# Kernel optimization log

Hardware: AMD Instinct MI355X
Metric: run time of the kernel (lower is better)

## Reference

```python
import jax, jax.numpy as jnp
import numpy as np

B, S, D = 4, 2048, 4096
E, R, OUT = 4, 64, 4096
NUM_MOD, NUM_REG, HID = 4, 3, 128
ALPHA = 128.0
SCALING = ALPHA / R  # alpha / rank = 2.0
BALANCE_COEFF = 0.01


def setup_inputs() -> dict:
    key = jax.random.key(0)
    ks = jax.random.split(key, 8)
    return {
        "x": jax.random.normal(ks[0], (B, S, D), jnp.float32),
        "reliability_vec": jax.random.uniform(ks[1], (B, NUM_MOD), jnp.float32),
        "regime_vec": jax.random.uniform(ks[2], (B, NUM_REG), jnp.float32),
        # LoRA experts stacked: A ~ N(0, 1/rank), B random (torch inits B=0; randomized here for a non-trivial baseline)
        "lora_A": jax.random.normal(ks[3], (E, R, D), jnp.float32) / np.sqrt(R).astype(np.float32),
        "lora_B": jax.random.normal(ks[4], (E, OUT, R), jnp.float32) * 0.02,
        # router: Linear(4103->128) -> GELU -> Linear(128->4)
        "w1": jax.random.normal(ks[5], (D + NUM_MOD + NUM_REG, HID), jnp.float32) * 0.02,
        "b1": jnp.zeros((HID,), jnp.float32),
        "w2": jax.random.normal(ks[6], (HID, E), jnp.float32) * 0.02,
        "b2": jnp.zeros((E,), jnp.float32),
    }


def reference(x, reliability_vec, regime_vec, lora_A, lora_B, w1, b1, w2, b2):
    # Router on pooled features + degradation context
    x_pooled = x.mean(axis=1)                                   # [B, D]
    router_in = jnp.concatenate([x_pooled, reliability_vec, regime_vec], axis=-1)
    h = jax.nn.gelu(router_in @ w1 + b1)                        # [B, HID]
    gate_logits = h @ w2 + b2                                   # [B, E]
    gate_probs = jax.nn.softmax(gate_logits, axis=-1)
    top_expert = jnp.argmax(gate_probs, axis=-1)                # [B] int

    # Sparse top-1 dispatch (eval path): gather each sample's expert weights
    A_sel = lora_A[top_expert]                                  # [B, R, D]
    B_sel = lora_B[top_expert]                                  # [B, OUT, R]
    xr = jnp.einsum('bsd,brd->bsr', x, A_sel)                   # [B, S, R]
    out = jnp.einsum('bsr,bor->bso', xr, B_sel) * SCALING       # [B, S, OUT]

    avg_gate = gate_probs.mean(axis=0)
    balance_loss = BALANCE_COEFF * (E * jnp.sum(avg_gate ** 2))
    return out, balance_loss
```

## Files before the change

### kernel.cpp

```cpp
#include <hip/hip_runtime.h>

constexpr int B_ = 4, S_ = 2048, D_ = 4096, E_ = 4, R_ = 64, OUT_ = 4096;
constexpr int NMOD = 4, NREG = 3, HID_ = 128;
constexpr int RIN_ = D_ + NMOD + NREG;
constexpr float SCALING_ = 2.0f;
constexpr int P_   = 128;
constexpr int KC_  = 33;

constexpr size_t WS_PP    = 0;
constexpr size_t WS_HACC2 = WS_PP + (size_t)P_ * B_ * D_;
constexpr size_t WS_TOP   = WS_HACC2 + B_ * KC_ * HID_;
constexpr size_t WS_APK   = WS_TOP + 16;
constexpr size_t WS_BPK   = WS_APK + (size_t)E_ * R_ * D_ / 2;

using short8 = __attribute__((ext_vector_type(8))) short;
using f32x4  = __attribute__((ext_vector_type(4))) float;
union frag_u { int4 i4; short8 s8; };

__device__ inline unsigned short f2bf(float f) {
    unsigned u = __float_as_uint(f);
    unsigned r = u + 0x7FFFu + ((u >> 16) & 1u);
    return (unsigned short)(r >> 16);
}

__global__ __launch_bounds__(256) void prep_kernel(const float* __restrict__ x,
                                                   const float* __restrict__ A,
                                                   const float* __restrict__ Bw,
                                                   float* __restrict__ pp,
                                                   ushort* __restrict__ Apk,
                                                   ushort* __restrict__ Bpk) {
    int bx = blockIdx.x, t = threadIdx.x;
    if (bx < 512) {
        int strip = bx >> 2, b = bx & 3;
        const float4* xp = (const float4*)(x + ((size_t)b * S_ + strip * 16) * D_);
        float4 a0 = {0,0,0,0}, a1 = {0,0,0,0}, a2 = {0,0,0,0}, a3 = {0,0,0,0};
#pragma unroll 4
        for (int r = 0; r < 16; ++r) {
            float4 v0 = xp[(size_t)r * 1024 + t];
            float4 v1 = xp[(size_t)r * 1024 + 256 + t];
            float4 v2 = xp[(size_t)r * 1024 + 512 + t];
            float4 v3 = xp[(size_t)r * 1024 + 768 + t];
            a0.x += v0.x; a0.y += v0.y; a0.z += v0.z; a0.w += v0.w;
            a1.x += v1.x; a1.y += v1.y; a1.z += v1.z; a1.w += v1.w;
            a2.x += v2.x; a2.y += v2.y; a2.z += v2.z; a2.w += v2.w;
            a3.x += v3.x; a3.y += v3.y; a3.z += v3.z; a3.w += v3.w;
        }
        float* ppb = pp + ((size_t)strip * B_ + b) * D_;
        *(float4*)&ppb[(t)       * 4] = a0;
        *(float4*)&ppb[(256 + t) * 4] = a1;
        *(float4*)&ppb[(512 + t) * 4] = a2;
        *(float4*)&ppb[(768 + t) * 4] = a3;
    } else if (bx < 1024) {
        int idx = (bx - 512) * 256 + t;
        int l = idx & 63, n = (idx >> 6) & 3, ks = (idx >> 8) & 127, e = idx >> 15;
        const float* src = A + ((size_t)e * R_ + n * 16 + (l & 15)) * D_
                             + ks * 32 + (l >> 4) * 8;
        float4 v0 = *(const float4*)(src);
        float4 v1 = *(const float4*)(src + 4);
        ushort* dst = Apk + (size_t)idx * 8;
        *(ushort4*)(dst)     = make_ushort4(f2bf(v0.x), f2bf(v0.y), f2bf(v0.z), f2bf(v0.w));
        *(ushort4*)(dst + 4) = make_ushort4(f2bf(v1.x), f2bf(v1.y), f2bf(v1.z), f2bf(v1.w));
    } else {
        int idx = (bx - 1024) * 256 + t;
        int l = idx & 63, kk = (idx >> 6) & 1, nt = (idx >> 7) & 255, e = idx >> 15;
        const float* src = Bw + ((size_t)e * OUT_ + nt * 16 + (l & 15)) * R_
                              + kk * 32 + (l >> 4) * 8;
        float4 v0 = *(const float4*)(src);
        float4 v1 = *(const float4*)(src + 4);
        ushort* dst = Bpk + (size_t)idx * 8;
        *(ushort4*)(dst)     = make_ushort4(f2bf(v0.x), f2bf(v0.y), f2bf(v0.z), f2bf(v0.w));
        *(ushort4*)(dst + 4) = make_ushort4(f2bf(v1.x), f2bf(v1.y), f2bf(v1.z), f2bf(v1.w));
    }
}

__global__ __launch_bounds__(256) void router_h_kernel(const float* __restrict__ pp,
                                                       const float* __restrict__ rel,
                                                       const float* __restrict__ reg,
                                                       const float* __restrict__ w1,
                                                       float* __restrict__ hacc2) {
    __shared__ float rin[128];
    __shared__ float red[256];
    int b = blockIdx.x, kc = blockIdx.y;
    int t = threadIdx.x;
    int k0 = kc * 128;
    {
        int k = k0 + (t & 127), half = t >> 7;
        float s = 0.f;
        if (k < D_) {
            for (int pi = half * 64; pi < half * 64 + 64; ++pi)
                s += pp[((size_t)pi * B_ + b) * D_ + k];
        }
        red[t] = s;
    }
    __syncthreads();
    if (t < 128) {
        int k = k0 + t;
        float v = 0.f;
        if (k < D_)               v = (red[t] + red[t + 128]) * (1.0f / S_);
        else if (k < D_ + NMOD)   v = rel[b * NMOD + (k - D_)];
        else if (k < RIN_)        v = reg[b * NREG + (k - D_ - NMOD)];
        rin[t] = v;
    }
    __syncthreads();
    int h = t & 127, half = t >> 7;
    float acc = 0.f;
#pragma unroll 8
    for (int i = 0; i < 64; ++i) {
        int kk = 2 * i + half;
        int k = k0 + kk;
        if (k < RIN_) acc += rin[kk] * w1[(size_t)k * HID_ + h];
    }
    red[t] = acc;
    __syncthreads();
    if (t < 128)
        hacc2[((size_t)b * KC_ + kc) * HID_ + t] = red[t] + red[t + 128];
}

__global__ void router_finish_kernel(const float* __restrict__ hacc2, const float* __restrict__ b1,
                                     const float* __restrict__ w2, const float* __restrict__ b2,
                                     int* __restrict__ top, float* __restrict__ bal_out) {
    __shared__ float h_lds[B_][HID_];
    __shared__ float logit[B_][E_];
    __shared__ float probs[B_][E_];
    int t = threadIdx.x;
    for (int b = 0; b < B_; ++b) {
        float v = b1[t];
        for (int j = 0; j < KC_; ++j) v += hacc2[((size_t)b * KC_ + j) * HID_ + t];
        float u = 0.7978845608028654f * (v + 0.044715f * v * v * v);
        h_lds[b][t] = 0.5f * v * (1.0f + tanhf(u));
    }
    __syncthreads();
    if (t < B_ * E_) {
        int b = t >> 2, e = t & 3;
        float acc = b2[e];
        for (int j = 0; j < HID_; ++j) acc += h_lds[b][j] * w2[j * E_ + e];
        logit[b][e] = acc;
    }
    __syncthreads();
    if (t < B_) {
        int b = t;
        float mx = logit[b][0]; int arg = 0;
        for (int e = 1; e < E_; ++e) if (logit[b][e] > mx) { mx = logit[b][e]; arg = e; }
        float s = 0.f, pv[E_];
        for (int e = 0; e < E_; ++e) { pv[e] = expf(logit[b][e] - mx); s += pv[e]; }
        for (int e = 0; e < E_; ++e) probs[b][e] = pv[e] / s;
        top[b] = arg;
    }
    __syncthreads();
    if (t == 0) {
        float bal = 0.f;
        for (int e = 0; e < E_; ++e) {
            float avg = 0.25f * (probs[0][e] + probs[1][e] + probs[2][e] + probs[3][e]);
            bal += avg * avg;
        }
        *bal_out = 0.01f * E_ * bal;
    }
}

__global__ __launch_bounds__(512) void xrout_kernel(const float* __restrict__ x,
                                                    const ushort* __restrict__ Apk,
                                                    const ushort* __restrict__ Bpk,
                                                    const int* __restrict__ top,
                                                    float* __restrict__ out) {
    __shared__ ushort xsw[8][16][70];
    __shared__ float  red[4][2][16][68];
    __shared__ ushort xs2[32][70];
    int sb = blockIdx.x, b = blockIdx.y;
    int e  = top[b];
    int s0 = sb * 32;
    int t = threadIdx.x, l = t & 63, w = t >> 6;
    int h = w & 1, ksl = w >> 1;
    int kb = ksl * 1024;

    const float* xb = x + ((size_t)b * S_ + s0 + h * 16) * D_;
    const int4*  ap = (const int4*)Apk + (size_t)e * 128 * 4 * 64 + l;
    f32x4 acc[4] = {};
    int lr = l >> 4, lc = l & 15;
    for (int i = 0; i < 16; ++i) {
        int k0 = kb + i * 64;
        float4 xv[4];
#pragma unroll
        for (int j = 0; j < 4; ++j)
            xv[j] = *(const float4*)(xb + (size_t)(lr + 4 * j) * D_ + k0 + lc * 4);
#pragma unroll
        for (int j = 0; j < 4; ++j)
            *(ushort4*)&xsw[w][lr + 4 * j][lc * 4] =
                make_ushort4(f2bf(xv[j].x), f2bf(xv[j].y), f2bf(xv[j].z), f2bf(xv[j].w));
#pragma unroll
        for (int kk = 0; kk < 2; ++kk) {
            short8 xf = *(const short8*)&xsw[w][l & 15][kk * 32 + (l >> 4) * 8];
            int ksg = ksl * 32 + i * 2 + kk;
#pragma unroll
            for (int n = 0; n < 4; ++n) {
                frag_u af; af.i4 = ap[((size_t)ksg * 4 + n) * 64];
                acc[n] = __builtin_amdgcn_mfma_f32_16x16x32_bf16(xf, af.s8, acc[n], 0, 0, 0);
            }
        }
    }
#pragma unroll
    for (int n = 0; n < 4; ++n)
#pragma unroll
        for (int i = 0; i < 4; ++i)
            red[ksl][h][(l >> 4) * 4 + i][n * 16 + (l & 15)] = acc[n][i];
    __syncthreads();
    {
        int row = t >> 4, c4 = (t & 15) * 4;
        int hh = row >> 4, r16 = row & 15;
        float4 s = *(const float4*)&red[0][hh][r16][c4];
#pragma unroll
        for (int ks = 1; ks < 4; ++ks) {
            float4 r = *(const float4*)&red[ks][hh][r16][c4];
            s.x += r.x; s.y += r.y; s.z += r.z; s.w += r.w;
        }
        *(ushort4*)&xs2[row][c4] = make_ushort4(f2bf(s.x), f2bf(s.y), f2bf(s.z), f2bf(s.w));
    }
    __syncthreads();

    short8 xf2[2][2];
#pragma unroll
    for (int m = 0; m < 2; ++m)
#pragma unroll
        for (int kk = 0; kk < 2; ++kk)
            xf2[m][kk] = *(const short8*)&xs2[m * 16 + (l & 15)][kk * 32 + (l >> 4) * 8];
    const int4* bp = (const int4*)Bpk + (size_t)e * 256 * 2 * 64 + l;
    float* ob = out + ((size_t)b * S_ + s0) * OUT_ + w * 512;
    int ro = (l >> 4) * 4, co = l & 15;
#pragma unroll 4
    for (int ntl = 0; ntl < 32; ++ntl) {
        int nt = w * 32 + ntl;
        frag_u bf0, bf1;
        bf0.i4 = bp[((size_t)nt * 2 + 0) * 64];
        bf1.i4 = bp[((size_t)nt * 2 + 1) * 64];
        f32x4 a2[2] = {};
#pragma unroll
        for (int m = 0; m < 2; ++m) {
            a2[m] = __builtin_amdgcn_mfma_f32_16x16x32_bf16(xf2[m][0], bf0.s8, a2[m], 0, 0, 0);
            a2[m] = __builtin_amdgcn_mfma_f32_16x16x32_bf16(xf2[m][1], bf1.s8, a2[m], 0, 0, 0);
        }
#pragma unroll
        for (int m = 0; m < 2; ++m)
#pragma unroll
            for (int i = 0; i < 4; ++i)
                ob[(size_t)(m * 16 + ro + i) * OUT_ + ntl * 16 + co] = a2[m][i] * SCALING_;
    }
}

extern "C" void kernel_launch(void* const* d_in, const int* in_sizes, int n_in,
                              void* d_out, int out_size, void* d_ws, size_t ws_size,
                              hipStream_t stream) {
    const float* x   = (const float*)d_in[0];
    const float* rel = (const float*)d_in[1];
    const float* reg = (const float*)d_in[2];
    const float* lA  = (const float*)d_in[3];
    const float* lB  = (const float*)d_in[4];
    const float* w1  = (const float*)d_in[5];
    const float* b1  = (const float*)d_in[6];
    const float* w2  = (const float*)d_in[7];
    const float* b2  = (const float*)d_in[8];
    float* out = (float*)d_out;
    float* ws  = (float*)d_ws;

    float*  pp    = ws + WS_PP;
    float*  hacc2 = ws + WS_HACC2;
    int*    top   = (int*)(ws + WS_TOP);
    ushort* Apk   = (ushort*)(ws + WS_APK);
    ushort* Bpk   = (ushort*)(ws + WS_BPK);

    prep_kernel<<<1536, 256, 0, stream>>>(x, lA, lB, pp, Apk, Bpk);
    router_h_kernel<<<dim3(B_, KC_), 256, 0, stream>>>(pp, rel, reg, w1, hacc2);
    router_finish_kernel<<<1, 128, 0, stream>>>(hacc2, b1, w2, b2, top,
                                                out + (size_t)out_size - 1);
    xrout_kernel<<<dim3(S_ / 32, B_), 512, 0, stream>>>(x, Apk, Bpk, top, out);
}
```

Before: 113.3 us.

## Shrink xrout row tile to 16 and split K across all eight waves

```diff
diff --git a/kernel.cpp b/kernel.cpp
--- a/kernel.cpp
+++ b/kernel.cpp
@@ -163,20 +163,19 @@
                                                     const int* __restrict__ top,
                                                     float* __restrict__ out) {
     __shared__ ushort xsw[8][16][70];
-    __shared__ float  red[4][2][16][68];
-    __shared__ ushort xs2[32][70];
+    __shared__ float  red[8][16][68];
+    __shared__ ushort xs2[16][70];
     int sb = blockIdx.x, b = blockIdx.y;
     int e  = top[b];
-    int s0 = sb * 32;
+    int s0 = sb * 16;
     int t = threadIdx.x, l = t & 63, w = t >> 6;
-    int h = w & 1, ksl = w >> 1;
-    int kb = ksl * 1024;
-
-    const float* xb = x + ((size_t)b * S_ + s0 + h * 16) * D_;
+    int kb = w * 512;
+
+    const float* xb = x + ((size_t)b * S_ + s0) * D_;
     const int4*  ap = (const int4*)Apk + (size_t)e * 128 * 4 * 64 + l;
     f32x4 acc[4] = {};
     int lr = l >> 4, lc = l & 15;
-    for (int i = 0; i < 16; ++i) {
+    for (int i = 0; i < 8; ++i) {
         int k0 = kb + i * 64;
         float4 xv[4];
 #pragma unroll
@@ -189,7 +188,7 @@
 #pragma unroll
         for (int kk = 0; kk < 2; ++kk) {
             short8 xf = *(const short8*)&xsw[w][l & 15][kk * 32 + (l >> 4) * 8];
-            int ksg = ksl * 32 + i * 2 + kk;
+            int ksg = w * 16 + i * 2 + kk;
 #pragma unroll
             for (int n = 0; n < 4; ++n) {
                 frag_u af; af.i4 = ap[((size_t)ksg * 4 + n) * 64];
@@ -201,27 +200,25 @@
     for (int n = 0; n < 4; ++n)
 #pragma unroll
         for (int i = 0; i < 4; ++i)
-            red[ksl][h][(l >> 4) * 4 + i][n * 16 + (l & 15)] = acc[n][i];
+            red[w][(l >> 4) * 4 + i][n * 16 + (l & 15)] = acc[n][i];
     __syncthreads();
     {
-        int row = t >> 4, c4 = (t & 15) * 4;
-        int hh = row >> 4, r16 = row & 15;
-        float4 s = *(const float4*)&red[0][hh][r16][c4];
-#pragma unroll
-        for (int ks = 1; ks < 4; ++ks) {
-            float4 r = *(const float4*)&red[ks][hh][r16][c4];
-            s.x += r.x; s.y += r.y; s.z += r.z; s.w += r.w;
-        }
-        *(ushort4*)&xs2[row][c4] = make_ushort4(f2bf(s.x), f2bf(s.y), f2bf(s.z), f2bf(s.w));
-    }
-    __syncthreads();
-
-    short8 xf2[2][2];
-#pragma unroll
-    for (int m = 0; m < 2; ++m)
-#pragma unroll
-        for (int kk = 0; kk < 2; ++kk)
-            xf2[m][kk] = *(const short8*)&xs2[m * 16 + (l & 15)][kk * 32 + (l >> 4) * 8];
+        int row = t >> 5, c2 = (t & 31) * 2;
+        float s0f = red[0][row][c2], s1f = red[0][row][c2 + 1];
+#pragma unroll
+        for (int ks = 1; ks < 8; ++ks) {
+            s0f += red[ks][row][c2];
+            s1f += red[ks][row][c2 + 1];
+        }
+        xs2[row][c2]     = f2bf(s0f);
+        xs2[row][c2 + 1] = f2bf(s1f);
+    }
+    __syncthreads();
+
+    short8 xf2[2];
+#pragma unroll
+    for (int kk = 0; kk < 2; ++kk)
+        xf2[kk] = *(const short8*)&xs2[l & 15][kk * 32 + (l >> 4) * 8];
     const int4* bp = (const int4*)Bpk + (size_t)e * 256 * 2 * 64 + l;
     float* ob = out + ((size_t)b * S_ + s0) * OUT_ + w * 512;
     int ro = (l >> 4) * 4, co = l & 15;
@@ -231,17 +228,12 @@
         frag_u bf0, bf1;
         bf0.i4 = bp[((size_t)nt * 2 + 0) * 64];
         bf1.i4 = bp[((size_t)nt * 2 + 1) * 64];
-        f32x4 a2[2] = {};
-#pragma unroll
-        for (int m = 0; m < 2; ++m) {
-            a2[m] = __builtin_amdgcn_mfma_f32_16x16x32_bf16(xf2[m][0], bf0.s8, a2[m], 0, 0, 0);
-            a2[m] = __builtin_amdgcn_mfma_f32_16x16x32_bf16(xf2[m][1], bf1.s8, a2[m], 0, 0, 0);
-        }
-#pragma unroll
-        for (int m = 0; m < 2; ++m)
-#pragma unroll
-            for (int i = 0; i < 4; ++i)
-                ob[(size_t)(m * 16 + ro + i) * OUT_ + ntl * 16 + co] = a2[m][i] * SCALING_;
+        f32x4 a2 = {};
+        a2 = __builtin_amdgcn_mfma_f32_16x16x32_bf16(xf2[0], bf0.s8, a2, 0, 0, 0);
+        a2 = __builtin_amdgcn_mfma_f32_16x16x32_bf16(xf2[1], bf1.s8, a2, 0, 0, 0);
+#pragma unroll
+        for (int i = 0; i < 4; ++i)
+            ob[(size_t)(ro + i) * OUT_ + ntl * 16 + co] = a2[i] * SCALING_;
     }
 }
 
@@ -270,5 +262,5 @@
     router_h_kernel<<<dim3(B_, KC_), 256, 0, stream>>>(pp, rel, reg, w1, hacc2);
     router_finish_kernel<<<1, 128, 0, stream>>>(hacc2, b1, w2, b2, top,
                                                 out + (size_t)out_size - 1);
-    xrout_kernel<<<dim3(S_ / 32, B_), 512, 0, stream>>>(x, Apk, Bpk, top, out);
-}
+    xrout_kernel<<<dim3(S_ / 16, B_), 512, 0, stream>>>(x, Apk, Bpk, top, out);
+}
```

Result: faster. 108.4 us (median of 2 runs) (-4.3%).
